# Kernel tuning notes

Measured on AMD Instinct MI355X. Metric: run time of the kernel, lower is better.

Reference implementation:

```python
import jax, jax.numpy as jnp
import numpy as np

D_MODEL = 2048
NUM_HEADS = 16
NUM_KV_HEADS = 4
HEAD_DIM = D_MODEL // NUM_HEADS  # 128
THETA = 10000.0


def _rotate_half(x):
    # interleaved rotate: pairs (x0,x1) -> (-x1, x0)
    x1 = x[..., ::2]
    x2 = x[..., 1::2]
    return jnp.stack((-x2, x1), axis=-1).reshape(x.shape)


def _rope_cos_sin(seq_len, dtype):
    inv_freq = 1.0 / (THETA ** (jnp.arange(0, HEAD_DIM, 2, dtype=jnp.float32) / HEAD_DIM))
    pos = jnp.arange(seq_len, dtype=jnp.float32)
    freqs = pos[:, None] * inv_freq[None, :]            # [S, HD/2]
    emb = jnp.repeat(freqs, 2, axis=-1)                  # [S, HD] interleaved
    return jnp.cos(emb).astype(dtype), jnp.sin(emb).astype(dtype)


def setup_inputs() -> dict:
    key = jax.random.key(0)
    ks = jax.random.split(key, 5)
    B, S = 2, 2048
    x = jax.random.normal(ks[0], (B, S, D_MODEL), dtype=jnp.float32)
    scale = 0.02
    wq = jax.random.normal(ks[1], (D_MODEL, NUM_HEADS * HEAD_DIM), dtype=jnp.float32) * scale
    wk = jax.random.normal(ks[2], (D_MODEL, NUM_KV_HEADS * HEAD_DIM), dtype=jnp.float32) * scale
    wv = jax.random.normal(ks[3], (D_MODEL, NUM_KV_HEADS * HEAD_DIM), dtype=jnp.float32) * scale
    wo = jax.random.normal(ks[4], (D_MODEL, D_MODEL), dtype=jnp.float32) * scale
    return {"x": x, "wq": wq, "wk": wk, "wv": wv, "wo": wo}


def reference(x, wq, wk, wv, wo):
    B, S, _ = x.shape
    q = (x @ wq).reshape(B, S, NUM_HEADS, HEAD_DIM).transpose(0, 2, 1, 3)      # [B,H,S,D]
    k = (x @ wk).reshape(B, S, NUM_KV_HEADS, HEAD_DIM).transpose(0, 2, 1, 3)   # [B,KV,S,D]
    v = (x @ wv).reshape(B, S, NUM_KV_HEADS, HEAD_DIM).transpose(0, 2, 1, 3)

    cos, sin = _rope_cos_sin(S, q.dtype)
    cos = cos[None, None]  # [1,1,S,HD]
    sin = sin[None, None]
    q = q * cos + _rotate_half(q) * sin
    k = k * cos + _rotate_half(k) * sin

    reps = NUM_HEADS // NUM_KV_HEADS
    k = jnp.repeat(k, reps, axis=1)  # [B,H,S,D]
    v = jnp.repeat(v, reps, axis=1)

    scale = 1.0 / jnp.sqrt(jnp.asarray(HEAD_DIM, dtype=q.dtype))
    scores = jnp.einsum('bhqd,bhkd->bhqk', q, k) * scale
    causal = jnp.tril(jnp.ones((S, S), dtype=bool))
    scores = jnp.where(causal[None, None], scores, jnp.finfo(scores.dtype).min)
    attn = jax.nn.softmax(scores, axis=-1)
    y = jnp.einsum('bhqk,bhkd->bhqd', attn, v)            # [B,H,S,D]
    y = y.transpose(0, 2, 1, 3).reshape(B, S, NUM_HEADS * HEAD_DIM)
    return y @ wo
```

## Files before the change

kernel.cpp:

```cpp
#include <hip/hip_runtime.h>
#include <hip/hip_bf16.h>
#include <stdint.h>

typedef __hip_bfloat16 bf16;
typedef __attribute__((ext_vector_type(8))) short short8;
typedef __attribute__((ext_vector_type(4))) float f32x4;

#define D_MODEL 2048
#define NHEADS 16
#define NKV 4
#define HD 128
#define BATCH 2
#define SEQ 2048
#define NTOK (BATCH*SEQ)
#define QKV_N 3072
#define QSCALE 0.08838834764831845f
#define QSCALE_L2E (0.08838834764831845f * 1.4426950408889634f)

__global__ __launch_bounds__(256) void trig_kernel(float2* __restrict__ tab) {
    int idx = blockIdx.x * 256 + threadIdx.x;
    int s = idx >> 6, i = idx & 63;
    double inv_freq = pow(10000.0, -(double)i / 64.0);
    double sn, cs;
    sincos((double)s * inv_freq, &sn, &cs);
    tab[idx] = make_float2((float)cs, (float)sn);
}

__global__ __launch_bounds__(256) void conv8(const float* __restrict__ in,
                                             bf16* __restrict__ out, int n8) {
    int idx = blockIdx.x * 256 + threadIdx.x;
    if (idx >= n8) return;
    const float4* p = (const float4*)(in + (size_t)idx * 8);
    float4 a = p[0], b = p[1];
    union { short8 v; bf16 e[8]; } u;
    u.e[0] = __float2bfloat16(a.x); u.e[1] = __float2bfloat16(a.y);
    u.e[2] = __float2bfloat16(a.z); u.e[3] = __float2bfloat16(a.w);
    u.e[4] = __float2bfloat16(b.x); u.e[5] = __float2bfloat16(b.y);
    u.e[6] = __float2bfloat16(b.z); u.e[7] = __float2bfloat16(b.w);
    *(short8*)(out + (size_t)idx * 8) = u.v;
}

#define TILE_LD 68
__global__ __launch_bounds__(256) void ct64(const float* __restrict__ in,
                                            bf16* __restrict__ out, int K, int N) {
    __shared__ float tile[64 * TILE_LD];
    int n0 = blockIdx.x * 64, k0 = blockIdx.y * 64;
    int t = threadIdx.x;
#pragma unroll
    for (int i = 0; i < 4; ++i) {
        int idx = t + 256 * i;
        int r = idx >> 4;
        int c4 = (idx & 15) * 4;
        *(float4*)&tile[r * TILE_LD + c4] = *(const float4*)(in + (size_t)(k0 + r) * N + n0 + c4);
    }
    __syncthreads();
#pragma unroll
    for (int i = 0; i < 2; ++i) {
        int idx = t + 256 * i;
        int n = idx >> 3;
        int kc = (idx & 7) * 8;
        union { short8 v; bf16 e[8]; } u;
#pragma unroll
        for (int j = 0; j < 8; ++j) u.e[j] = __float2bfloat16(tile[(kc + j) * TILE_LD + n]);
        *(short8*)(out + (size_t)(n0 + n) * K + k0 + kc) = u.v;
    }
}

__global__ __launch_bounds__(256) void vt64(const bf16* __restrict__ qkvb,
                                            bf16* __restrict__ vT) {
    __shared__ bf16 tile[64 * 72];
    int vd0 = blockIdx.x * 64, s0 = blockIdx.y * 64, b = blockIdx.z;
    int t = threadIdx.x;
#pragma unroll
    for (int i = 0; i < 2; ++i) {
        int idx = t + 256 * i;
        int r = idx >> 3;
        int c8 = (idx & 7) * 8;
        *(int4*)&tile[r * 72 + c8] =
            *(const int4*)(qkvb + (size_t)(b * SEQ + s0 + r) * QKV_N + 2560 + vd0 + c8);
    }
    __syncthreads();
#pragma unroll
    for (int i = 0; i < 2; ++i) {
        int idx = t + 256 * i;
        int vd = idx >> 3;
        int s8 = (idx & 7) * 8;
        union { short8 v; bf16 e[8]; } u;
#pragma unroll
        for (int j = 0; j < 8; ++j) u.e[j] = tile[(s8 + j) * 72 + vd];
        *(short8*)(vT + (size_t)(b * 512 + vd0 + vd) * 2048 + s0 + s8) = u.v;
    }
}

template <typename OutT, bool ROPE>
__global__ __launch_bounds__(256) void gemm_bt(const bf16* __restrict__ A,
                                               const bf16* __restrict__ Bt,
                                               OutT* __restrict__ C, int M, int N, int K,
                                               const float2* __restrict__ trig) {
    __shared__ bf16 As[128 * 32];
    __shared__ bf16 Bs[128 * 32];
    const int GX = gridDim.x;
    const int nwg = GX * gridDim.y;
    const int lin = blockIdx.y * GX + blockIdx.x;
    const int swz = (lin & 7) * (nwg >> 3) + (lin >> 3);
    const int m0 = (swz / GX) * 128, n0 = (swz % GX) * 128;
    const int tid = threadIdx.x;
    const int wave = tid >> 6, lane = tid & 63;
    const int wr = wave >> 1, wc = wave & 1;
    const int l15 = lane & 15, g = lane >> 4;
    const int srow = lane >> 2;
    const int sk8 = (lane & 3) * 8;
    f32x4 acc[4][4] = {};

    for (int k0 = 0; k0 < K; k0 += 32) {
        __syncthreads();
#pragma unroll
        for (int i = 0; i < 2; ++i) {
            int chunk = wave * 2 + i;
            const bf16* ga = A + (size_t)(m0 + chunk * 16 + srow) * K + k0 + sk8;
            bf16* la = As + chunk * 512 + lane * 8;
            __builtin_amdgcn_global_load_lds((const __attribute__((address_space(1))) void*)ga,
                                             (__attribute__((address_space(3))) void*)la, 16, 0, 0);
            const bf16* gb = Bt + (size_t)(n0 + chunk * 16 + srow) * K + k0 + sk8;
            bf16* lb = Bs + chunk * 512 + lane * 8;
            __builtin_amdgcn_global_load_lds((const __attribute__((address_space(1))) void*)gb,
                                             (__attribute__((address_space(3))) void*)lb, 16, 0, 0);
        }
        __syncthreads();
        short8 af[4], bfr[4];
#pragma unroll
        for (int mi = 0; mi < 4; ++mi)
            af[mi] = *(const short8*)&As[(wr * 64 + mi * 16 + l15) * 32 + g * 8];
#pragma unroll
        for (int ni = 0; ni < 4; ++ni)
            bfr[ni] = *(const short8*)&Bs[(wc * 64 + ni * 16 + l15) * 32 + g * 8];
#pragma unroll
        for (int mi = 0; mi < 4; ++mi)
#pragma unroll
            for (int ni = 0; ni < 4; ++ni)
                acc[mi][ni] = __builtin_amdgcn_mfma_f32_16x16x32_bf16(af[mi], bfr[ni], acc[mi][ni], 0, 0, 0);
    }
#pragma unroll
    for (int mi = 0; mi < 4; ++mi)
#pragma unroll
        for (int ni = 0; ni < 4; ++ni) {
            int row = m0 + wr * 64 + mi * 16 + g * 4;
            int col = n0 + wc * 64 + ni * 16 + l15;
#pragma unroll
            for (int r = 0; r < 4; ++r) {
                float v = acc[mi][ni][r];
                if constexpr (ROPE) {
                    float partner = __shfl_xor(v, 1);
                    if (col < 2560) {
                        int s = (row + r) & (SEQ - 1);
                        int i2 = (col & 127) >> 1;
                        float2 t = trig[s * 64 + i2];
                        v = (col & 1) ? (v * t.x + partner * t.y)
                                      : (v * t.x - partner * t.y);
                    }
                    if (col < 2048) v *= QSCALE_L2E;
                }
                if constexpr (__is_same(OutT, float))
                    C[(size_t)(row + r) * N + col] = v;
                else
                    C[(size_t)(row + r) * N + col] = __float2bfloat16(v);
            }
        }
}

#define PL_LD 72
__global__ __launch_bounds__(256) void attn9(const bf16* __restrict__ qkv,
                                             const bf16* __restrict__ vT,
                                             bf16* __restrict__ y) {
    const int bx = blockIdx.x, h = blockIdx.y, b = blockIdx.z;
    const int kvh = h >> 2;
    const int tid = threadIdx.x, wave = tid >> 6, lane = tid & 63;
    const int l15 = lane & 15, g = lane >> 4;
    __shared__ bf16 Ks[64 * 128];
    __shared__ bf16 Vt[128 * 64];
    __shared__ bf16 Pl[4][16 * PL_LD];
    bf16* plw = Pl[0] + wave * 16 * PL_LD;

    for (int half = 0; half < 2; ++half) {
        const int qt = half ? (31 - bx) : bx;
        const int qrow0 = qt * 64 + wave * 16;
        short8 qf[4];
        {
            const bf16* qp = qkv + (size_t)(b * SEQ + qrow0 + l15) * QKV_N + h * HD + g * 8;
#pragma unroll
            for (int c = 0; c < 4; ++c) qf[c] = *(const short8*)(qp + c * 32);
        }
        f32x4 acc[8] = {};
        float m_[4], lsum[4];
#pragma unroll
        for (int r = 0; r < 4; ++r) { m_[r] = -3.0e38f; lsum[r] = 0.f; }

        const bf16* gk[4];
        const bf16* gv[4];
#pragma unroll
        for (int i = 0; i < 4; ++i) {
            int cidx = tid + 256 * i;
            int key = cidx >> 4, j = cidx & 15;
            gk[i] = qkv + (size_t)(b * SEQ + key) * QKV_N + D_MODEL + kvh * HD + 8 * (j ^ (key & 7));
            int d = cidx >> 3, j2 = cidx & 7;
            gv[i] = vT + (size_t)(b * 512 + kvh * HD + d) * 2048 + 8 * (j2 ^ (d & 7));
        }

        const int diag_kv0 = qt * 64;
        for (int kv0 = 0; kv0 <= diag_kv0; kv0 += 64) {
#pragma unroll
            for (int i = 0; i < 4; ++i) {
                int cidx = tid + 256 * i;
                __builtin_amdgcn_global_load_lds(
                    (const __attribute__((address_space(1))) void*)gk[i],
                    (__attribute__((address_space(3))) void*)(Ks + cidx * 8), 16, 0, 0);
                __builtin_amdgcn_global_load_lds(
                    (const __attribute__((address_space(1))) void*)gv[i],
                    (__attribute__((address_space(3))) void*)(Vt + cidx * 8), 16, 0, 0);
                gk[i] += 64 * QKV_N;
                gv[i] += 64;
            }
            __syncthreads();

            f32x4 sc[4];
#pragma unroll
            for (int ct = 0; ct < 4; ++ct) {
                sc[ct] = (f32x4){0.f, 0.f, 0.f, 0.f};
                int key = ct * 16 + l15;
                int ksw = (key & 7) << 3;
#pragma unroll
                for (int c = 0; c < 4; ++c) {
                    short8 kf = *(const short8*)&Ks[key * 128 + ((c * 32 + g * 8) ^ ksw)];
                    sc[ct] = __builtin_amdgcn_mfma_f32_16x16x32_bf16(qf[c], kf, sc[ct], 0, 0, 0);
                }
            }
            if (kv0 == diag_kv0) {
                int qbase = qrow0 + g * 4;
#pragma unroll
                for (int ct = 0; ct < 4; ++ct) {
                    int key = kv0 + ct * 16 + l15;
#pragma unroll
                    for (int r = 0; r < 4; ++r)
                        if (key > qbase + r) sc[ct][r] = -3.0e38f;
                }
            }
#pragma unroll
            for (int r = 0; r < 4; ++r) {
                float mx = fmaxf(fmaxf(sc[0][r], sc[1][r]), fmaxf(sc[2][r], sc[3][r]));
#pragma unroll
                for (int o = 1; o < 16; o <<= 1) mx = fmaxf(mx, __shfl_xor(mx, o));
                if (mx > m_[r] + 8.0f) {
                    float alpha = exp2f(m_[r] - mx);
                    m_[r] = mx;
                    lsum[r] *= alpha;
#pragma unroll
                    for (int nt = 0; nt < 8; ++nt) acc[nt][r] *= alpha;
                }
                float p0 = exp2f(sc[0][r] - m_[r]);
                float p1 = exp2f(sc[1][r] - m_[r]);
                float p2 = exp2f(sc[2][r] - m_[r]);
                float p3 = exp2f(sc[3][r] - m_[r]);
                int row = g * 4 + r;
                plw[row * PL_LD + l15]      = __float2bfloat16(p0);
                plw[row * PL_LD + 16 + l15] = __float2bfloat16(p1);
                plw[row * PL_LD + 32 + l15] = __float2bfloat16(p2);
                plw[row * PL_LD + 48 + l15] = __float2bfloat16(p3);
                lsum[r] += (p0 + p1) + (p2 + p3);
            }
            short8 pf0 = *(const short8*)&plw[l15 * PL_LD + g * 8];
            short8 pf1 = *(const short8*)&plw[l15 * PL_LD + 32 + g * 8];
#pragma unroll
            for (int nt = 0; nt < 8; ++nt) {
                int d = nt * 16 + l15;
                int dsw = (d & 7) << 3;
                short8 vf0 = *(const short8*)&Vt[d * 64 + ((g * 8) ^ dsw)];
                short8 vf1 = *(const short8*)&Vt[d * 64 + ((32 + g * 8) ^ dsw)];
                acc[nt] = __builtin_amdgcn_mfma_f32_16x16x32_bf16(pf0, vf0, acc[nt], 0, 0, 0);
                acc[nt] = __builtin_amdgcn_mfma_f32_16x16x32_bf16(pf1, vf1, acc[nt], 0, 0, 0);
            }
            __syncthreads();
        }
        float linv[4];
#pragma unroll
        for (int r = 0; r < 4; ++r) {
            float ls = lsum[r];
#pragma unroll
            for (int o = 1; o < 16; o <<= 1) ls += __shfl_xor(ls, o);
            linv[r] = 1.0f / ls;
        }
        int qrow = qrow0 + g * 4;
#pragma unroll
        for (int nt = 0; nt < 8; ++nt) {
            int d = nt * 16 + l15;
#pragma unroll
            for (int r = 0; r < 4; ++r)
                y[(size_t)(b * SEQ + qrow + r) * D_MODEL + h * HD + d] =
                    __float2bfloat16(acc[nt][r] * linv[r]);
        }
        __syncthreads();
    }
}

extern "C" void kernel_launch(void* const* d_in, const int* in_sizes, int n_in,
                              void* d_out, int out_size, void* d_ws, size_t ws_size,
                              hipStream_t stream) {
    const float* x  = (const float*)d_in[0];
    const float* wq = (const float*)d_in[1];
    const float* wk = (const float*)d_in[2];
    const float* wv = (const float*)d_in[3];
    const float* wo = (const float*)d_in[4];

    bf16*   qkvb  = (bf16*)d_ws;
    bf16*   ybb   = (bf16*)d_ws + (size_t)NTOK * 3072;
    bf16*   woT   = (bf16*)d_ws + (size_t)NTOK * 3072 + (size_t)NTOK * D_MODEL;
    bf16*   xb    = (bf16*)d_out;
    bf16*   wqkvT = (bf16*)d_out + (size_t)NTOK * D_MODEL;
    float2* trig  = (float2*)((bf16*)d_out + (size_t)NTOK * D_MODEL + (size_t)QKV_N * D_MODEL);
    bf16*   vT    = (bf16*)d_out;
    float*  outf  = (float*)d_out;

    conv8<<<dim3(NTOK * D_MODEL / (256 * 8)), 256, 0, stream>>>(x, xb, NTOK * D_MODEL / 8);
    ct64<<<dim3(32, 32), 256, 0, stream>>>(wq, wqkvT, 2048, 2048);
    ct64<<<dim3(8, 32), 256, 0, stream>>>(wk, wqkvT + (size_t)2048 * 2048, 2048, 512);
    ct64<<<dim3(8, 32), 256, 0, stream>>>(wv, wqkvT + (size_t)2560 * 2048, 2048, 512);
    ct64<<<dim3(32, 32), 256, 0, stream>>>(wo, woT, 2048, 2048);
    trig_kernel<<<dim3(SEQ * 64 / 256), 256, 0, stream>>>(trig);

    gemm_bt<bf16, true><<<dim3(QKV_N / 128, NTOK / 128), 256, 0, stream>>>(
        xb, wqkvT, qkvb, NTOK, QKV_N, D_MODEL, trig);

    vt64<<<dim3(8, 32, BATCH), 256, 0, stream>>>(qkvb, vT);

    attn9<<<dim3(16, NHEADS, BATCH), 256, 0, stream>>>(qkvb, vT, ybb);

    gemm_bt<float, false><<<dim3(D_MODEL / 128, NTOK / 128), 256, 0, stream>>>(
        ybb, woT, outf, NTOK, D_MODEL, D_MODEL, nullptr);
}
```

Baseline: 265.0 us.

## Double GEMM K-tile to 64 with XOR-swizzled LDS layout

The GEMM main loop now stages 64-wide K slices of A and B into LDS instead of 32, which halves the number of barrier pairs per output tile. The LDS layout is XOR-swizzled on the source side so that the direct-to-LDS loads land in a permuted column order, meant to avoid bank conflicts on the fragment reads. Global pointers are precomputed once and advanced each iteration. LDS use doubles to 32 KB per block, which may lower occupancy.

```diff
diff --git a/kernel.cpp b/kernel.cpp
--- a/kernel.cpp
+++ b/kernel.cpp
@@ -97,8 +97,8 @@
                                                const bf16* __restrict__ Bt,
                                                OutT* __restrict__ C, int M, int N, int K,
                                                const float2* __restrict__ trig) {
-    __shared__ bf16 As[128 * 32];
-    __shared__ bf16 Bs[128 * 32];
+    __shared__ bf16 As[128 * 64];
+    __shared__ bf16 Bs[128 * 64];
     const int GX = gridDim.x;
     const int nwg = GX * gridDim.y;
     const int lin = blockIdx.y * GX + blockIdx.x;
@@ -108,37 +108,53 @@
     const int wave = tid >> 6, lane = tid & 63;
     const int wr = wave >> 1, wc = wave & 1;
     const int l15 = lane & 15, g = lane >> 4;
-    const int srow = lane >> 2;
-    const int sk8 = (lane & 3) * 8;
     f32x4 acc[4][4] = {};
 
-    for (int k0 = 0; k0 < K; k0 += 32) {
+    const bf16* ga[4];
+    const bf16* gb[4];
+#pragma unroll
+    for (int i = 0; i < 4; ++i) {
+        int cidx = tid + 256 * i;
+        int r = cidx >> 3, j = cidx & 7;
+        int sc = 8 * (j ^ (r & 7));
+        ga[i] = A + (size_t)(m0 + r) * K + sc;
+        gb[i] = Bt + (size_t)(n0 + r) * K + sc;
+    }
+
+    for (int k0 = 0; k0 < K; k0 += 64) {
         __syncthreads();
 #pragma unroll
-        for (int i = 0; i < 2; ++i) {
-            int chunk = wave * 2 + i;
-            const bf16* ga = A + (size_t)(m0 + chunk * 16 + srow) * K + k0 + sk8;
-            bf16* la = As + chunk * 512 + lane * 8;
-            __builtin_amdgcn_global_load_lds((const __attribute__((address_space(1))) void*)ga,
-                                             (__attribute__((address_space(3))) void*)la, 16, 0, 0);
-            const bf16* gb = Bt + (size_t)(n0 + chunk * 16 + srow) * K + k0 + sk8;
-            bf16* lb = Bs + chunk * 512 + lane * 8;
-            __builtin_amdgcn_global_load_lds((const __attribute__((address_space(1))) void*)gb,
-                                             (__attribute__((address_space(3))) void*)lb, 16, 0, 0);
+        for (int i = 0; i < 4; ++i) {
+            int cidx = tid + 256 * i;
+            __builtin_amdgcn_global_load_lds(
+                (const __attribute__((address_space(1))) void*)ga[i],
+                (__attribute__((address_space(3))) void*)(As + cidx * 8), 16, 0, 0);
+            __builtin_amdgcn_global_load_lds(
+                (const __attribute__((address_space(1))) void*)gb[i],
+                (__attribute__((address_space(3))) void*)(Bs + cidx * 8), 16, 0, 0);
+            ga[i] += 64;
+            gb[i] += 64;
         }
         __syncthreads();
-        short8 af[4], bfr[4];
-#pragma unroll
-        for (int mi = 0; mi < 4; ++mi)
-            af[mi] = *(const short8*)&As[(wr * 64 + mi * 16 + l15) * 32 + g * 8];
-#pragma unroll
-        for (int ni = 0; ni < 4; ++ni)
-            bfr[ni] = *(const short8*)&Bs[(wc * 64 + ni * 16 + l15) * 32 + g * 8];
-#pragma unroll
-        for (int mi = 0; mi < 4; ++mi)
-#pragma unroll
-            for (int ni = 0; ni < 4; ++ni)
-                acc[mi][ni] = __builtin_amdgcn_mfma_f32_16x16x32_bf16(af[mi], bfr[ni], acc[mi][ni], 0, 0, 0);
+#pragma unroll
+        for (int kk = 0; kk < 2; ++kk) {
+            short8 af[4], bfr[4];
+#pragma unroll
+            for (int mi = 0; mi < 4; ++mi) {
+                int row = wr * 64 + mi * 16 + l15;
+                af[mi] = *(const short8*)&As[row * 64 + ((kk * 32 + g * 8) ^ ((row & 7) << 3))];
+            }
+#pragma unroll
+            for (int ni = 0; ni < 4; ++ni) {
+                int row = wc * 64 + ni * 16 + l15;
+                bfr[ni] = *(const short8*)&Bs[row * 64 + ((kk * 32 + g * 8) ^ ((row & 7) << 3))];
+            }
+#pragma unroll
+            for (int mi = 0; mi < 4; ++mi)
+#pragma unroll
+                for (int ni = 0; ni < 4; ++ni)
+                    acc[mi][ni] = __builtin_amdgcn_mfma_f32_16x16x32_bf16(af[mi], bfr[ni], acc[mi][ni], 0, 0, 0);
+        }
     }
 #pragma unroll
     for (int mi = 0; mi < 4; ++mi)
```

Result: no change. 270.3 us (+2.0%).
